# Optimization experiments

Hardware: AMD Instinct MI355X
Metric: run time of the kernel (lower is better)

Reference implementation:

```python
import jax, jax.numpy as jnp
import numpy as np

B, S, D = 2, 2048, 1024
H, HKV = 16, 4
HD = D // H          # 64
NREP = H // HKV      # 4
EPS = 1e-6
ROPE_BASE = 10000.0


def setup_inputs() -> dict:
    key = jax.random.key(0)
    ks = jax.random.split(key, 6)
    std = 0.02
    return {
        "x": jax.random.normal(ks[0], (B, S, D), dtype=jnp.float32),
        "Wq": jax.random.normal(ks[1], (D, H * HD), dtype=jnp.float32) * std,
        "Wk": jax.random.normal(ks[2], (D, HKV * HD), dtype=jnp.float32) * std,
        "Wv": jax.random.normal(ks[3], (D, HKV * HD), dtype=jnp.float32) * std,
        "Wo": jax.random.normal(ks[4], (D, D), dtype=jnp.float32) * std,
        "norm_w": jnp.ones((D,), dtype=jnp.float32),
    }


def _rope_cos_sin(seq_len, head_dim, dtype):
    inv_freq = 1.0 / (ROPE_BASE ** (jnp.arange(0, head_dim, 2, dtype=jnp.float32) / head_dim))
    t = jnp.arange(seq_len, dtype=jnp.float32)
    freqs = jnp.outer(t, inv_freq)                 # [S, HD/2]
    emb = jnp.concatenate([freqs, freqs], axis=-1)  # [S, HD]
    return jnp.cos(emb).astype(dtype), jnp.sin(emb).astype(dtype)


def _rotate_half(x):
    x1, x2 = jnp.split(x, 2, axis=-1)
    return jnp.concatenate([-x2, x1], axis=-1)


def _apply_rope(x, cos, sin):
    # x: [B, nh, S, HD]; cos/sin: [S, HD]
    return x * cos[None, None] + _rotate_half(x) * sin[None, None]


def reference(x, Wq, Wk, Wv, Wo, norm_w):
    b, s, _ = x.shape
    q = (x @ Wq).reshape(b, s, H, HD).transpose(0, 2, 1, 3)      # [B,H,S,HD]
    k = (x @ Wk).reshape(b, s, HKV, HD).transpose(0, 2, 1, 3)    # [B,HKV,S,HD]
    v = (x @ Wv).reshape(b, s, HKV, HD).transpose(0, 2, 1, 3)

    cos, sin = _rope_cos_sin(s, HD, x.dtype)
    q = _apply_rope(q, cos, sin)
    k = _apply_rope(k, cos, sin)

    # repeat kv heads to match q heads
    k = jnp.repeat(k, NREP, axis=1)   # [B,H,S,HD]
    v = jnp.repeat(v, NREP, axis=1)

    scale = HD ** -0.5
    scores = jnp.einsum('bhqd,bhkd->bhqk', q, k) * scale   # [B,H,S,S]
    attn = jax.nn.softmax(scores, axis=-1)
    out = jnp.einsum('bhqk,bhkd->bhqd', attn, v)            # [B,H,S,HD]
    out = out.transpose(0, 2, 1, 3).reshape(b, s, D)
    out = out @ Wo

    # RMSNorm
    rms = jnp.sqrt(jnp.mean(out * out, axis=-1, keepdims=True) + EPS)
    out = out / rms * norm_w
    return out
```

## Files before the change

### kernel.cpp

```cpp
#include <hip/hip_runtime.h>
#include <hip/hip_bf16.h>
#include <stdint.h>
#include <math.h>

typedef __bf16 bf16x8 __attribute__((ext_vector_type(8)));
typedef float f32x4 __attribute__((ext_vector_type(4)));
typedef float f32x16 __attribute__((ext_vector_type(16)));

#define B_    2
#define S_    2048
#define D_    1024
#define H_    16
#define HKV_  4
#define HD_   64
#define MTOT  4096
#define NQKV  1536
#define BHS   65536

#define ZERO16 {0.f,0.f,0.f,0.f,0.f,0.f,0.f,0.f,0.f,0.f,0.f,0.f,0.f,0.f,0.f,0.f}

__device__ __forceinline__ unsigned short f2bf(float f) {
  union { float f; unsigned u; } v; v.f = f;
  unsigned r = (v.u + 0x7FFFu + ((v.u >> 16) & 1u)) >> 16;
  return (unsigned short)r;
}

__device__ __forceinline__ float bf2f(unsigned short u) {
  union { unsigned u; float f; } v; v.u = (unsigned)u << 16; return v.f;
}

__device__ __forceinline__ float fast_exp2(float x) {
  return __builtin_amdgcn_exp2f(x);
}

__device__ __forceinline__ unsigned cvt_pk_bf16(float lo, float hi) {
  unsigned r;
  asm("v_cvt_pk_bf16_f32 %0, %1, %2" : "=v"(r) : "v"(lo), "v"(hi));
  return r;
}

__device__ __forceinline__ void gl_lds16(const void* g, void* l) {
  __builtin_amdgcn_global_load_lds((const __attribute__((address_space(1))) void*)g,
                                   (__attribute__((address_space(3))) void*)l, 16, 0, 0);
}

__global__ __launch_bounds__(256) void k_pre(const float* __restrict__ Wq, const float* __restrict__ Wk,
                                             const float* __restrict__ Wv, const float* __restrict__ Wo,
                                             const float* __restrict__ x,
                                             unsigned short* __restrict__ wqkvt,
                                             unsigned short* __restrict__ wot,
                                             unsigned short* __restrict__ xb,
                                             float* __restrict__ cost, float* __restrict__ sint) {
  int bid = blockIdx.x, tid = threadIdx.x;
  if (bid < 640) {
    const float* src; unsigned short* dst; int ldsrc, cb, rb;
    if (bid < 256)      { src = Wq; dst = wqkvt;                          ldsrc = 1024; cb = (bid & 15) * 64; rb = (bid >> 4) * 64; }
    else if (bid < 320) { int i = bid - 256; src = Wk; dst = wqkvt + (size_t)1024 * 1024; ldsrc = 256; cb = (i & 3) * 64; rb = (i >> 2) * 64; }
    else if (bid < 384) { int i = bid - 320; src = Wv; dst = wqkvt + (size_t)1280 * 1024; ldsrc = 256; cb = (i & 3) * 64; rb = (i >> 2) * 64; }
    else                { int i = bid - 384; src = Wo; dst = wot;         ldsrc = 1024; cb = (i & 15) * 64; rb = (i >> 4) * 64; }
    __shared__ unsigned short T[64][72];
    for (int rep = 0; rep < 4; ++rep) {
      int idx = rep * 256 + tid;
      int r = idx >> 4, seg = idx & 15;
      float4 v = *(const float4*)&src[(size_t)(rb + r) * ldsrc + cb + seg * 4];
      T[seg*4+0][r] = f2bf(v.x);
      T[seg*4+1][r] = f2bf(v.y);
      T[seg*4+2][r] = f2bf(v.z);
      T[seg*4+3][r] = f2bf(v.w);
    }
    __syncthreads();
    for (int rep = 0; rep < 2; ++rep) {
      int idx = rep * 256 + tid;
      int c = idx >> 3, seg = idx & 7;
      *(uint4*)&dst[(size_t)(cb + c) * 1024 + rb + seg * 8] = *(const uint4*)&T[c][seg * 8];
    }
  } else if (bid < 896) {
    int idx = (bid - 640) * 256 + tid;
    int s = idx >> 5, i = idx & 31;
    double inv = exp(-(double)i / 32.0 * log(10000.0));
    double ang = (double)s * inv;
    cost[idx] = (float)cos(ang);
    sint[idx] = (float)sin(ang);
  } else {
    int i = (bid - 896) * 256 + tid;
    const int n4 = MTOT * D_ / 4;
    for (; i < n4; i += 1024 * 256) {
      float4 v = ((const float4*)x)[i];
      ushort4 o;
      o.x = f2bf(v.x); o.y = f2bf(v.y); o.z = f2bf(v.z); o.w = f2bf(v.w);
      ((ushort4*)xb)[i] = o;
    }
  }
}

__global__ __launch_bounds__(256) void k_gemm_qkv(const unsigned short* __restrict__ A,
                                                  const unsigned short* __restrict__ Bt,
                                                  const float* __restrict__ cost,
                                                  const float* __restrict__ sint,
                                                  unsigned short* __restrict__ Qb,
                                                  unsigned short* __restrict__ Kb,
                                                  unsigned short* __restrict__ Vt) {
  int nb = blockIdx.x, mb = blockIdx.y;
  __shared__ unsigned short Arena[12288];
  unsigned short* ArA = Arena;
  unsigned short* ArB = Arena + 4096;
  int tid = threadIdx.x, lane = tid & 63, w = tid >> 6;
  int wr = w >> 1, wc = w & 1;
  f32x4 acc[2][4];
  for (int m = 0; m < 2; ++m) for (int n = 0; n < 4; ++n) acc[m][n] = (f32x4){0.f, 0.f, 0.f, 0.f};

  const int r16 = lane >> 2;
  const int c8  = (lane & 3) * 8;

  auto stage = [&](int buf, int kt) {
    gl_lds16(&A[(size_t)(mb * 64 + w * 16 + r16) * D_ + kt * 32 + c8], &ArA[buf * 2048 + w * 512]);
    for (int j = 0; j < 2; ++j)
      gl_lds16(&Bt[(size_t)(nb * 128 + w * 32 + j * 16 + r16) * D_ + kt * 32 + c8],
               &ArB[buf * 4096 + (w * 32 + j * 16) * 32]);
  };
  stage(0, 0);
  const int NT = D_ / 32;
  int cur = 0;
  const int lr = lane & 15, lg8 = (lane >> 4) * 8;
  for (int kt = 0; kt < NT; ++kt) {
    __syncthreads();
    if (kt + 1 < NT) stage(cur ^ 1, kt + 1);
    bf16x8 af[2], bfr[4];
    for (int m = 0; m < 2; ++m) af[m]  = *(const bf16x8*)&ArA[cur * 2048 + (wr * 32 + m * 16 + lr) * 32 + lg8];
    for (int n = 0; n < 4; ++n) bfr[n] = *(const bf16x8*)&ArB[cur * 4096 + (wc * 64 + n * 16 + lr) * 32 + lg8];
    for (int m = 0; m < 2; ++m)
      for (int n = 0; n < 4; ++n)
        acc[m][n] = __builtin_amdgcn_mfma_f32_16x16x32_bf16(af[m], bfr[n], acc[m][n], 0, 0, 0);
    cur ^= 1;
  }

  const int lq = (lane >> 4) * 4;
  const int b = mb >> 5;
  const int s0 = (mb & 31) * 64;

  if (nb < 10) {
    const float QSCALE = 0.18033688011112042f;
    float scl = (nb < 8) ? QSCALE : 1.f;
    #pragma unroll
    for (int m = 0; m < 2; ++m) {
      #pragma unroll
      for (int n = 0; n < 4; ++n) {
        int gc = nb * 128 + wc * 64 + n * 16 + lr;
        int d  = gc & 63, d2 = d & 31;
        float sgn = (d < 32) ? -1.f : 1.f;
        unsigned short* dst;
        if (nb < 8) {
          int h = gc >> 6;
          dst = Qb + (((size_t)(b * H_ + h)) * S_) * HD_ + d;
        } else {
          int hk = (gc - 1024) >> 6;
          dst = Kb + (((size_t)(b * HKV_ + hk)) * S_) * HD_ + d;
        }
        #pragma unroll
        for (int r = 0; r < 4; ++r) {
          int s = s0 + wr * 32 + m * 16 + lq + r;
          float c  = cost[s * 32 + d2];
          float sn = sint[s * 32 + d2];
          float xv = acc[m][n][r];
          float xp = acc[m][n ^ 2][r];
          float o = (xv * c + sgn * xp * sn) * scl;
          dst[(size_t)s * HD_] = f2bf(o);
        }
      }
    }
  } else {
    __syncthreads();
    #pragma unroll
    for (int m = 0; m < 2; ++m)
      #pragma unroll
      for (int n = 0; n < 4; ++n)
        #pragma unroll
        for (int r = 0; r < 4; ++r) {
          int c = wc * 64 + n * 16 + lr;
          int rw = wr * 32 + m * 16 + lq + r;
          Arena[c * 72 + rw] = f2bf(acc[m][n][r]);
        }
    __syncthreads();
    {
      int j = tid >> 1, q = tid & 1;
      int v_off = (nb - 10) * 128 + j;
      int hk = v_off >> 6, dl = v_off & 63;
      unsigned short* dst = Vt + (((size_t)(b * HKV_ + hk)) * HD_ + dl) * S_ + s0 + q * 32;
      const unsigned short* srcp = &Arena[j * 72 + q * 32];
      #pragma unroll
      for (int k2 = 0; k2 < 4; ++k2)
        *(uint4*)&dst[k2 * 8] = *(const uint4*)&srcp[k2 * 8];
    }
  }
}

__global__ __launch_bounds__(256) void k_gemm_bt(const unsigned short* __restrict__ A,
                                                 const unsigned short* __restrict__ Bt,
                                                 unsigned short* __restrict__ C0,
                                                 unsigned short* __restrict__ C1,
                                                 int M, int N, int Kfull) {
  int nb = blockIdx.x, mb = blockIdx.y, z = blockIdx.z;
  int kbase = z * (Kfull >> 1);
  int Klen = Kfull >> 1;
  unsigned short* C = z ? C1 : C0;
  __shared__ unsigned short ArA[2][64 * 32];
  __shared__ unsigned short ArB[2][128 * 32];
  int tid = threadIdx.x, lane = tid & 63, w = tid >> 6;
  int wr = w >> 1, wc = w & 1;
  f32x4 acc[2][4];
  for (int m = 0; m < 2; ++m) for (int n = 0; n < 4; ++n) acc[m][n] = (f32x4){0.f, 0.f, 0.f, 0.f};

  const int r16 = lane >> 2;
  const int c8  = (lane & 3) * 8;

  auto stage = [&](int buf, int kt) {
    gl_lds16(&A[(size_t)(mb * 64 + w * 16 + r16) * Kfull + kbase + kt * 32 + c8], &ArA[buf][w * 512]);
    for (int j = 0; j < 2; ++j)
      gl_lds16(&Bt[(size_t)(nb * 128 + w * 32 + j * 16 + r16) * Kfull + kbase + kt * 32 + c8],
               &ArB[buf][(w * 32 + j * 16) * 32]);
  };
  stage(0, 0);
  int NT = Klen / 32;
  int cur = 0;
  const int lr = lane & 15, lg8 = (lane >> 4) * 8;
  for (int kt = 0; kt < NT; ++kt) {
    __syncthreads();
    if (kt + 1 < NT) stage(cur ^ 1, kt + 1);
    bf16x8 af[2], bfr[4];
    for (int m = 0; m < 2; ++m) af[m]  = *(const bf16x8*)&ArA[cur][(wr * 32 + m * 16 + lr) * 32 + lg8];
    for (int n = 0; n < 4; ++n) bfr[n] = *(const bf16x8*)&ArB[cur][(wc * 64 + n * 16 + lr) * 32 + lg8];
    for (int m = 0; m < 2; ++m)
      for (int n = 0; n < 4; ++n)
        acc[m][n] = __builtin_amdgcn_mfma_f32_16x16x32_bf16(af[m], bfr[n], acc[m][n], 0, 0, 0);
    cur ^= 1;
  }
  int lq = (lane >> 4) * 4;
  for (int m = 0; m < 2; ++m)
    for (int n = 0; n < 4; ++n)
      for (int r = 0; r < 4; ++r)
        C[(size_t)(mb * 64 + wr * 32 + m * 16 + lq + r) * N + nb * 128 + wc * 64 + n * 16 + lr] =
            f2bf(acc[m][n][r]);
}

__global__ __launch_bounds__(512, 2) void k_attn(const unsigned short* __restrict__ Q,
                                                 const unsigned short* __restrict__ K,
                                                 const unsigned short* __restrict__ Vt,
                                                 unsigned short* __restrict__ Ob) {
  int wg = ((blockIdx.x & 7) << 6) | (blockIdx.x >> 3);
  int qt = wg & 15;
  int bh = wg >> 4;
  int b = bh >> 4, h = bh & 15, hk = h >> 2;
  const unsigned short* Qp = Q + (((size_t)(b * H_ + h)) * S_ + qt * 128) * HD_;
  const unsigned short* Kp = K + ((size_t)(b * HKV_ + hk)) * S_ * HD_;
  const unsigned short* Vp = Vt + ((size_t)(b * HKV_ + hk)) * HD_ * S_;

  __shared__ unsigned short Lds[2 * 16384];

  const int tid = threadIdx.x, lane = tid & 63, w = tid >> 6;
  const int g  = w >> 2;
  const int wl = w & 3;
  const int col = lane & 31;
  const int hi  = lane >> 5;
  const int sw  = lane & 7;
  const int kv0 = g * (S_ / 2);
  const int gbase = g * 16384;

  const unsigned short* pka[4];
  #pragma unroll
  for (int kc = 0; kc < 4; ++kc)
    pka[kc] = &Lds[gbase + col * 64 + ((kc * 2 + hi) ^ sw) * 8];

  bf16x8 qf[4];
  {
    const unsigned short* qrow = Qp + (size_t)(wl * 32 + col) * HD_;
    #pragma unroll
    for (int dc = 0; dc < 4; ++dc)
      qf[dc] = *(const bf16x8*)&qrow[dc * 16 + hi * 8];
  }

  union { unsigned short s[8]; bf16x8 v; } onesu;
  #pragma unroll
  for (int i = 0; i < 8; ++i) onesu.s[i] = 0x3F80;
  const bf16x8 ones = onesu.v;

  f32x16 oacc0 = ZERO16, oacc1 = ZERO16, lacc = ZERO16;

  const int rl = lane >> 3, cs = lane & 7;
  const int row0 = wl * 16 + rl;
  const int csrc = (cs ^ (row0 & 7)) * 8;
  const unsigned short* srcK = &Kp[(size_t)(kv0 + row0) * HD_ + csrc];
  const unsigned short* srcV = &Vp[(size_t)row0 * S_ + kv0 + csrc];

  auto stage = [&](int be) {
    gl_lds16(srcK,           &Lds[gbase + be + (wl * 16) * 64]);
    gl_lds16(srcK + 8 * HD_, &Lds[gbase + be + (wl * 16 + 8) * 64]);
    gl_lds16(srcV,           &Lds[gbase + be + 8192 + (wl * 16) * 64]);
    gl_lds16(srcV + 8 * S_,  &Lds[gbase + be + 8192 + (wl * 16 + 8) * 64]);
    srcK += 64 * HD_;
    srcV += 64;
  };

  auto compute = [&](int be) {
    bf16x8 pf[4];
    #pragma unroll
    for (int blk2 = 0; blk2 < 2; ++blk2) {
      f32x16 st = ZERO16;
      __builtin_amdgcn_s_setprio(1);
      #pragma unroll
      for (int kc = 0; kc < 4; ++kc) {
        bf16x8 kf = *(const bf16x8*)(pka[kc] + be + blk2 * 2048);
        st = __builtin_amdgcn_mfma_f32_32x32x16_bf16(kf, qf[kc], st, 0, 0, 0);
      }
      __builtin_amdgcn_s_setprio(0);
      #pragma unroll
      for (int i = 0; i < 16; ++i)
        st[i] = fast_exp2(st[i]);
      #pragma unroll
      for (int kcl = 0; kcl < 2; ++kcl) {
        int base = kcl * 8;
        unsigned u0 = cvt_pk_bf16(st[base + 0], st[base + 1]);
        unsigned u1 = cvt_pk_bf16(st[base + 2], st[base + 3]);
        unsigned u2 = cvt_pk_bf16(st[base + 4], st[base + 5]);
        unsigned u3 = cvt_pk_bf16(st[base + 6], st[base + 7]);
        asm("v_permlane32_swap_b32 %0, %1" : "+v"(u0), "+v"(u2));
        asm("v_permlane32_swap_b32 %0, %1" : "+v"(u1), "+v"(u3));
        union { unsigned u[4]; bf16x8 v; } pk;
        pk.u[0] = u0; pk.u[1] = u1; pk.u[2] = u2; pk.u[3] = u3;
        pf[blk2 * 2 + kcl] = pk.v;
      }
    }
    __builtin_amdgcn_s_setprio(1);
    #pragma unroll
    for (int kc = 0; kc < 4; ++kc)
      lacc = __builtin_amdgcn_mfma_f32_32x32x16_bf16(ones, pf[kc], lacc, 0, 0, 0);
    #pragma unroll
    for (int kc = 0; kc < 4; ++kc) {
      bf16x8 v0 = *(const bf16x8*)(pka[kc] + be + 8192);
      bf16x8 v1 = *(const bf16x8*)(pka[kc] + be + 8192 + 2048);
      oacc0 = __builtin_amdgcn_mfma_f32_32x32x16_bf16(v0, pf[kc], oacc0, 0, 0, 0);
      oacc1 = __builtin_amdgcn_mfma_f32_32x32x16_bf16(v1, pf[kc], oacc1, 0, 0, 0);
    }
    __builtin_amdgcn_s_setprio(0);
  };

  stage(0);
  for (int it = 0; it < 8; ++it) {
    __syncthreads();
    stage(4096);
    compute(0);
    __syncthreads();
    if (it < 7) stage(0);
    compute(4096);
  }

  __syncthreads();
  float* xch = (float*)Lds;
  if (g == 0) {
    float* slot = xch + ((size_t)wl * 64 + lane) * 33;
    #pragma unroll
    for (int i = 0; i < 16; ++i) { slot[i] = oacc0[i]; slot[16 + i] = oacc1[i]; }
    slot[32] = lacc[0];
  }
  __syncthreads();
  if (g == 1) {
    const float* slot = xch + ((size_t)wl * 64 + lane) * 33;
    float rinv = 1.f / (lacc[0] + slot[32]);
    int qrow = qt * 128 + wl * 32 + col;
    unsigned short* ob = Ob + ((size_t)(b * S_ + qrow)) * D_ + h * 64;
    #pragma unroll
    for (int rr = 0; rr < 4; ++rr) {
      ushort4 o0, o1;
      o0.x = f2bf((oacc0[rr*4+0] + slot[rr*4+0]) * rinv);
      o0.y = f2bf((oacc0[rr*4+1] + slot[rr*4+1]) * rinv);
      o0.z = f2bf((oacc0[rr*4+2] + slot[rr*4+2]) * rinv);
      o0.w = f2bf((oacc0[rr*4+3] + slot[rr*4+3]) * rinv);
      o1.x = f2bf((oacc1[rr*4+0] + slot[16+rr*4+0]) * rinv);
      o1.y = f2bf((oacc1[rr*4+1] + slot[16+rr*4+1]) * rinv);
      o1.z = f2bf((oacc1[rr*4+2] + slot[16+rr*4+2]) * rinv);
      o1.w = f2bf((oacc1[rr*4+3] + slot[16+rr*4+3]) * rinv);
      *(ushort4*)&ob[8 * rr + 4 * hi]      = o0;
      *(ushort4*)&ob[32 + 8 * rr + 4 * hi] = o1;
    }
  }
}

__global__ __launch_bounds__(256) void k_rmsnorm(const unsigned short* __restrict__ in0,
                                                 const unsigned short* __restrict__ in1,
                                                 const float* __restrict__ wt,
                                                 float* __restrict__ out) {
  int row = blockIdx.x, tid = threadIdx.x;
  ushort4 u0 = *(const ushort4*)&in0[(size_t)row * D_ + tid * 4];
  ushort4 u1 = *(const ushort4*)&in1[(size_t)row * D_ + tid * 4];
  float x0 = bf2f(u0.x) + bf2f(u1.x);
  float x1 = bf2f(u0.y) + bf2f(u1.y);
  float x2 = bf2f(u0.z) + bf2f(u1.z);
  float x3 = bf2f(u0.w) + bf2f(u1.w);
  float ss = x0 * x0 + x1 * x1 + x2 * x2 + x3 * x3;
  for (int o = 32; o >= 1; o >>= 1) ss += __shfl_xor(ss, o);
  __shared__ float red[4];
  if ((tid & 63) == 0) red[tid >> 6] = ss;
  __syncthreads();
  float tot = red[0] + red[1] + red[2] + red[3];
  float rinv = 1.f / sqrtf(tot * (1.f / 1024.f) + 1e-6f);
  float4 wv = ((const float4*)wt)[tid];
  float4 o;
  o.x = x0 * rinv * wv.x;
  o.y = x1 * rinv * wv.y;
  o.z = x2 * rinv * wv.z;
  o.w = x3 * rinv * wv.w;
  ((float4*)(out + (size_t)row * D_))[tid] = o;
}

extern "C" void kernel_launch(void* const* d_in, const int* in_sizes, int n_in,
                              void* d_out, int out_size, void* d_ws, size_t ws_size,
                              hipStream_t stream) {
  const float* x  = (const float*)d_in[0];
  const float* Wq = (const float*)d_in[1];
  const float* Wk = (const float*)d_in[2];
  const float* Wv = (const float*)d_in[3];
  const float* Wo = (const float*)d_in[4];
  const float* nw = (const float*)d_in[5];
  float* out = (float*)d_out;

  char* p = (char*)d_ws;
  unsigned short* xb    = (unsigned short*)p; p += (size_t)MTOT * D_ * 2;
  char*           slot  = p;                  p += (size_t)18 * 1024 * 1024;
  unsigned short* wqkvt = (unsigned short*)p; p += (size_t)NQKV * D_ * 2;
  unsigned short* wot   = (unsigned short*)p; p += (size_t)D_ * D_ * 2;
  unsigned short* qb    = (unsigned short*)p; p += (size_t)B_ * H_ * S_ * HD_ * 2;
  unsigned short* kb    = (unsigned short*)p; p += (size_t)B_ * HKV_ * S_ * HD_ * 2;
  unsigned short* vtb   = (unsigned short*)p; p += (size_t)B_ * HKV_ * HD_ * S_ * 2;
  char*           big2  = p;                  p += (size_t)MTOT * D_ * 2 * 2;
  float*          mlold = (float*)p;          p += (size_t)2 * BHS * 4;
  float*          cost  = (float*)p;          p += (size_t)S_ * 32 * 4;
  float*          sint  = (float*)p;          p += (size_t)S_ * 32 * 4;
  (void)mlold;

  unsigned short* attnb   = (unsigned short*)big2;
  unsigned short* proj_p0 = (unsigned short*)slot;
  unsigned short* proj_p1 = (unsigned short*)(slot + (size_t)MTOT * D_ * 2);

  k_pre<<<1920, 256, 0, stream>>>(Wq, Wk, Wv, Wo, x, wqkvt, wot, xb, cost, sint);

  k_gemm_qkv<<<dim3(NQKV / 128, MTOT / 64), 256, 0, stream>>>(xb, wqkvt, cost, sint, qb, kb, vtb);
  k_attn<<<512, 512, 0, stream>>>(qb, kb, vtb, attnb);
  k_gemm_bt<<<dim3(D_ / 128, MTOT / 64, 2), 256, 0, stream>>>(attnb, wot, proj_p0, proj_p1, MTOT, D_, D_);
  k_rmsnorm<<<MTOT, 256, 0, stream>>>(proj_p0, proj_p1, nw, out);
}
```

Measured before the change: 102.2 us.

## Widen GEMM K-tiles with XOR-swizzled LDS and compute softmax row sums on VALU

Both GEMM kernels now stage 64-wide K tiles with an XOR swizzle on LDS columns, which halves the loop trip count and barriers and aims to avoid bank conflicts on the fragment reads. Shared memory per block doubles. In attention, the row-sum MFMA against a ones vector is replaced by scalar accumulation of the exp values plus a cross-lane shuffle, which frees matrix-core work at the cost of extra VALU adds. The row sum is now taken from fp32 exp values rather than the bf16-rounded probabilities, which slightly changes the normalization.

```diff
diff --git a/kernel.cpp b/kernel.cpp
--- a/kernel.cpp
+++ b/kernel.cpp
@@ -101,36 +101,40 @@
                                                   unsigned short* __restrict__ Kb,
                                                   unsigned short* __restrict__ Vt) {
   int nb = blockIdx.x, mb = blockIdx.y;
-  __shared__ unsigned short Arena[12288];
-  unsigned short* ArA = Arena;
-  unsigned short* ArB = Arena + 4096;
+  __shared__ unsigned short Arena[2][12288];
   int tid = threadIdx.x, lane = tid & 63, w = tid >> 6;
   int wr = w >> 1, wc = w & 1;
   f32x4 acc[2][4];
   for (int m = 0; m < 2; ++m) for (int n = 0; n < 4; ++n) acc[m][n] = (f32x4){0.f, 0.f, 0.f, 0.f};
 
-  const int r16 = lane >> 2;
-  const int c8  = (lane & 3) * 8;
+  const int rl = lane >> 3;
+  const int csw = ((lane & 7) ^ rl) * 8;
 
   auto stage = [&](int buf, int kt) {
-    gl_lds16(&A[(size_t)(mb * 64 + w * 16 + r16) * D_ + kt * 32 + c8], &ArA[buf * 2048 + w * 512]);
     for (int j = 0; j < 2; ++j)
-      gl_lds16(&Bt[(size_t)(nb * 128 + w * 32 + j * 16 + r16) * D_ + kt * 32 + c8],
-               &ArB[buf * 4096 + (w * 32 + j * 16) * 32]);
+      gl_lds16(&A[(size_t)(mb * 64 + w * 16 + j * 8 + rl) * D_ + kt * 64 + csw],
+               &Arena[buf][(w * 16 + j * 8) * 64]);
+    for (int j = 0; j < 4; ++j)
+      gl_lds16(&Bt[(size_t)(nb * 128 + w * 32 + j * 8 + rl) * D_ + kt * 64 + csw],
+               &Arena[buf][4096 + (w * 32 + j * 8) * 64]);
   };
   stage(0, 0);
-  const int NT = D_ / 32;
+  const int NT = D_ / 64;
   int cur = 0;
-  const int lr = lane & 15, lg8 = (lane >> 4) * 8;
+  const int lr = lane & 15, lg = lane >> 4, swl = lane & 7;
   for (int kt = 0; kt < NT; ++kt) {
     __syncthreads();
     if (kt + 1 < NT) stage(cur ^ 1, kt + 1);
-    bf16x8 af[2], bfr[4];
-    for (int m = 0; m < 2; ++m) af[m]  = *(const bf16x8*)&ArA[cur * 2048 + (wr * 32 + m * 16 + lr) * 32 + lg8];
-    for (int n = 0; n < 4; ++n) bfr[n] = *(const bf16x8*)&ArB[cur * 4096 + (wc * 64 + n * 16 + lr) * 32 + lg8];
-    for (int m = 0; m < 2; ++m)
-      for (int n = 0; n < 4; ++n)
-        acc[m][n] = __builtin_amdgcn_mfma_f32_16x16x32_bf16(af[m], bfr[n], acc[m][n], 0, 0, 0);
+    #pragma unroll
+    for (int kk = 0; kk < 2; ++kk) {
+      int ch = ((kk * 4 + lg) ^ swl) * 8;
+      bf16x8 af[2], bfr[4];
+      for (int m = 0; m < 2; ++m) af[m]  = *(const bf16x8*)&Arena[cur][(wr * 32 + m * 16 + lr) * 64 + ch];
+      for (int n = 0; n < 4; ++n) bfr[n] = *(const bf16x8*)&Arena[cur][4096 + (wc * 64 + n * 16 + lr) * 64 + ch];
+      for (int m = 0; m < 2; ++m)
+        for (int n = 0; n < 4; ++n)
+          acc[m][n] = __builtin_amdgcn_mfma_f32_16x16x32_bf16(af[m], bfr[n], acc[m][n], 0, 0, 0);
+    }
     cur ^= 1;
   }
 
@@ -170,6 +174,7 @@
     }
   } else {
     __syncthreads();
+    unsigned short* T = &Arena[0][0];
     #pragma unroll
     for (int m = 0; m < 2; ++m)
       #pragma unroll
@@ -178,7 +183,7 @@
         for (int r = 0; r < 4; ++r) {
           int c = wc * 64 + n * 16 + lr;
           int rw = wr * 32 + m * 16 + lq + r;
-          Arena[c * 72 + rw] = f2bf(acc[m][n][r]);
+          T[c * 72 + rw] = f2bf(acc[m][n][r]);
         }
     __syncthreads();
     {
@@ -186,7 +191,7 @@
       int v_off = (nb - 10) * 128 + j;
       int hk = v_off >> 6, dl = v_off & 63;
       unsigned short* dst = Vt + (((size_t)(b * HKV_ + hk)) * HD_ + dl) * S_ + s0 + q * 32;
-      const unsigned short* srcp = &Arena[j * 72 + q * 32];
+      const unsigned short* srcp = &T[j * 72 + q * 32];
       #pragma unroll
       for (int k2 = 0; k2 < 4; ++k2)
         *(uint4*)&dst[k2 * 8] = *(const uint4*)&srcp[k2 * 8];
@@ -203,35 +208,40 @@
   int kbase = z * (Kfull >> 1);
   int Klen = Kfull >> 1;
   unsigned short* C = z ? C1 : C0;
-  __shared__ unsigned short ArA[2][64 * 32];
-  __shared__ unsigned short ArB[2][128 * 32];
+  __shared__ unsigned short Arena[2][12288];
   int tid = threadIdx.x, lane = tid & 63, w = tid >> 6;
   int wr = w >> 1, wc = w & 1;
   f32x4 acc[2][4];
   for (int m = 0; m < 2; ++m) for (int n = 0; n < 4; ++n) acc[m][n] = (f32x4){0.f, 0.f, 0.f, 0.f};
 
-  const int r16 = lane >> 2;
-  const int c8  = (lane & 3) * 8;
+  const int rl = lane >> 3;
+  const int csw = ((lane & 7) ^ rl) * 8;
 
   auto stage = [&](int buf, int kt) {
-    gl_lds16(&A[(size_t)(mb * 64 + w * 16 + r16) * Kfull + kbase + kt * 32 + c8], &ArA[buf][w * 512]);
     for (int j = 0; j < 2; ++j)
-      gl_lds16(&Bt[(size_t)(nb * 128 + w * 32 + j * 16 + r16) * Kfull + kbase + kt * 32 + c8],
-               &ArB[buf][(w * 32 + j * 16) * 32]);
+      gl_lds16(&A[(size_t)(mb * 64 + w * 16 + j * 8 + rl) * Kfull + kbase + kt * 64 + csw],
+               &Arena[buf][(w * 16 + j * 8) * 64]);
+    for (int j = 0; j < 4; ++j)
+      gl_lds16(&Bt[(size_t)(nb * 128 + w * 32 + j * 8 + rl) * Kfull + kbase + kt * 64 + csw],
+               &Arena[buf][4096 + (w * 32 + j * 8) * 64]);
   };
   stage(0, 0);
-  int NT = Klen / 32;
+  int NT = Klen / 64;
   int cur = 0;
-  const int lr = lane & 15, lg8 = (lane >> 4) * 8;
+  const int lr = lane & 15, lg = lane >> 4, swl = lane & 7;
   for (int kt = 0; kt < NT; ++kt) {
     __syncthreads();
     if (kt + 1 < NT) stage(cur ^ 1, kt + 1);
-    bf16x8 af[2], bfr[4];
-    for (int m = 0; m < 2; ++m) af[m]  = *(const bf16x8*)&ArA[cur][(wr * 32 + m * 16 + lr) * 32 + lg8];
-    for (int n = 0; n < 4; ++n) bfr[n] = *(const bf16x8*)&ArB[cur][(wc * 64 + n * 16 + lr) * 32 + lg8];
-    for (int m = 0; m < 2; ++m)
-      for (int n = 0; n < 4; ++n)
-        acc[m][n] = __builtin_amdgcn_mfma_f32_16x16x32_bf16(af[m], bfr[n], acc[m][n], 0, 0, 0);
+    #pragma unroll
+    for (int kk = 0; kk < 2; ++kk) {
+      int ch = ((kk * 4 + lg) ^ swl) * 8;
+      bf16x8 af[2], bfr[4];
+      for (int m = 0; m < 2; ++m) af[m]  = *(const bf16x8*)&Arena[cur][(wr * 32 + m * 16 + lr) * 64 + ch];
+      for (int n = 0; n < 4; ++n) bfr[n] = *(const bf16x8*)&Arena[cur][4096 + (wc * 64 + n * 16 + lr) * 64 + ch];
+      for (int m = 0; m < 2; ++m)
+        for (int n = 0; n < 4; ++n)
+          acc[m][n] = __builtin_amdgcn_mfma_f32_16x16x32_bf16(af[m], bfr[n], acc[m][n], 0, 0, 0);
+    }
     cur ^= 1;
   }
   int lq = (lane >> 4) * 4;
@@ -278,12 +288,8 @@
       qf[dc] = *(const bf16x8*)&qrow[dc * 16 + hi * 8];
   }
 
-  union { unsigned short s[8]; bf16x8 v; } onesu;
-  #pragma unroll
-  for (int i = 0; i < 8; ++i) onesu.s[i] = 0x3F80;
-  const bf16x8 ones = onesu.v;
-
-  f32x16 oacc0 = ZERO16, oacc1 = ZERO16, lacc = ZERO16;
+  f32x16 oacc0 = ZERO16, oacc1 = ZERO16;
+  float l_run = 0.f;
 
   const int rl = lane >> 3, cs = lane & 7;
   const int row0 = wl * 16 + rl;
@@ -302,6 +308,7 @@
 
   auto compute = [&](int be) {
     bf16x8 pf[4];
+    float ps0 = 0.f, ps1 = 0.f, ps2 = 0.f, ps3 = 0.f;
     #pragma unroll
     for (int blk2 = 0; blk2 < 2; ++blk2) {
       f32x16 st = ZERO16;
@@ -313,8 +320,13 @@
       }
       __builtin_amdgcn_s_setprio(0);
       #pragma unroll
-      for (int i = 0; i < 16; ++i)
-        st[i] = fast_exp2(st[i]);
+      for (int i = 0; i < 16; i += 4) {
+        st[i]     = fast_exp2(st[i]);
+        st[i + 1] = fast_exp2(st[i + 1]);
+        st[i + 2] = fast_exp2(st[i + 2]);
+        st[i + 3] = fast_exp2(st[i + 3]);
+        ps0 += st[i]; ps1 += st[i + 1]; ps2 += st[i + 2]; ps3 += st[i + 3];
+      }
       #pragma unroll
       for (int kcl = 0; kcl < 2; ++kcl) {
         int base = kcl * 8;
@@ -329,10 +341,10 @@
         pf[blk2 * 2 + kcl] = pk.v;
       }
     }
+    float psum = (ps0 + ps1) + (ps2 + ps3);
+    psum += __shfl_xor(psum, 32);
+    l_run += psum;
     __builtin_amdgcn_s_setprio(1);
-    #pragma unroll
-    for (int kc = 0; kc < 4; ++kc)
-      lacc = __builtin_amdgcn_mfma_f32_32x32x16_bf16(ones, pf[kc], lacc, 0, 0, 0);
     #pragma unroll
     for (int kc = 0; kc < 4; ++kc) {
       bf16x8 v0 = *(const bf16x8*)(pka[kc] + be + 8192);
@@ -359,12 +371,12 @@
     float* slot = xch + ((size_t)wl * 64 + lane) * 33;
     #pragma unroll
     for (int i = 0; i < 16; ++i) { slot[i] = oacc0[i]; slot[16 + i] = oacc1[i]; }
-    slot[32] = lacc[0];
+    slot[32] = l_run;
   }
   __syncthreads();
   if (g == 1) {
     const float* slot = xch + ((size_t)wl * 64 + lane) * 33;
-    float rinv = 1.f / (lacc[0] + slot[32]);
+    float rinv = 1.f / (l_run + slot[32]);
     int qrow = qt * 128 + wl * 32 + col;
     unsigned short* ob = Ob + ((size_t)(b * S_ + qrow)) * D_ + h * 64;
     #pragma unroll
```

Result: faster. 94.12 us (-8.0%).
